# Optimization experiments

Measured on AMD Instinct MI355X. Metric: run time of the kernel, lower is better.

## Reference

```python
import jax, jax.numpy as jnp
import numpy as np


def forward_warp_bilinear(im0, flow):
    # im0: [B,C,H,W], flow: [B,H,W,2] (flow[...,0]=dx, flow[...,1]=dy)
    B, C, H, W = im0.shape
    HW = H * W
    xg = jnp.arange(W, dtype=im0.dtype)
    yg = jnp.arange(H, dtype=im0.dtype)
    x = xg[None, None, :] + flow[..., 0]  # [B,H,W] target x
    y = yg[None, :, None] + flow[..., 1]  # [B,H,W] target y
    x0 = jnp.floor(x)
    y0 = jnp.floor(y)
    x1 = x0 + 1.0
    y1 = y0 + 1.0
    # bilinear splat weights for the 4 neighbours
    w_nw = (x1 - x) * (y1 - y)
    w_ne = (x - x0) * (y1 - y)
    w_sw = (x1 - x) * (y - y0)
    w_se = (x - x0) * (y - y0)
    corners = [(x0, y0, w_nw), (x1, y0, w_ne), (x0, y1, w_sw), (x1, y1, w_se)]
    idx_list, wgt_list = [], []
    for cx, cy, cw in corners:
        xi = cx.astype(jnp.int32)
        yi = cy.astype(jnp.int32)
        valid = (xi >= 0) & (xi < W) & (yi >= 0) & (yi < H)
        flat = jnp.clip(yi, 0, H - 1) * W + jnp.clip(xi, 0, W - 1)  # [B,H,W]
        idx_list.append(flat.reshape(B, HW))
        wgt_list.append(jnp.where(valid, cw, 0.0).reshape(B, HW))
    idx = jnp.concatenate(idx_list, axis=1)  # [B,4*HW]
    wgt = jnp.concatenate(wgt_list, axis=1)  # [B,4*HW]
    src = im0.reshape(B, C, 1, HW)  # source values, tiled over corners
    vals = (src * wgt.reshape(B, 1, 4, HW)).reshape(B, C, 4 * HW)

    def scatter_one(v, i):  # v: [C,4*HW], i: [4*HW]
        return jnp.zeros((C, HW), dtype=v.dtype).at[:, i].add(v)

    out = jax.vmap(scatter_one)(vals, idx)  # [B,C,HW]
    return out.reshape(B, C, H, W)


def setup_inputs() -> dict:
    key = jax.random.key(0)
    k1, k2 = jax.random.split(key)
    B, C, H, W = 8, 16, 512, 512
    im0 = jax.random.normal(k1, (B, C, H, W), dtype=jnp.float32)
    flow = jax.random.normal(k2, (B, H, W, 2), dtype=jnp.float32) * 8.0
    return {"im0": im0, "flow": flow}


def reference(im0, flow):
    return forward_warp_bilinear(im0, flow)
```

## Files before the change

kernel.cpp:

```cpp
#include <hip/hip_runtime.h>


constexpr int B = 8;
constexpr int C = 16;
constexpr int H = 512;
constexpr int W = 512;
constexpr int HW = H * W;

constexpr int T    = 16;
constexpr int R    = 32;
constexpr int TX   = W / T;
constexpr int TY   = H / T;
constexpr int NTILE = B * TX * TY;
constexpr int LCAP = 768;
constexpr int VSTAGE = 400;
constexpr int FARCAP = 1 << 16;
constexpr int NCELL = 289;
constexpr float FARTH = 30.0f;

constexpr size_t WS_CNT  = 0;
constexpr size_t WS_FCNT = 32768;
constexpr size_t WS_FLST = 32896;
constexpr size_t WS_LIST = WS_FLST + (size_t)FARCAP * 8;
constexpr size_t WS_IMT  = (WS_LIST + (size_t)NTILE * LCAP * 2 + 255) & ~(size_t)255;
constexpr size_t IMT_BYTES = (size_t)B * HW * C * 4;

template <bool CL>
__global__ __launch_bounds__(256) void fwarp_prep(
    const float* __restrict__ im0,
    const float* __restrict__ flow,
    float* __restrict__ imT,
    int* __restrict__ cnt,
    int* __restrict__ farcnt,
    int2* __restrict__ farlist,
    unsigned short* __restrict__ list) {

  __shared__ float t[256 * 17];
  const int blk = blockIdx.x;
  const int b   = blk >> 10;
  const int p0  = (blk & 1023) * 256;
  const int tid = threadIdx.x;
  const int lane = tid & 63;
  const int p   = p0 + tid;
  const int idx = (b << 18) + p;

  float v[16];
  if (CL) {
    const float* src = im0 + (size_t)b * C * HW + p0;
    #pragma unroll
    for (int c = 0; c < C; ++c) v[c] = src[(size_t)c * HW + tid];
  }

  float2 f = reinterpret_cast<const float2*>(flow)[idx];
  const int hh = p >> 9, ww = p & (W - 1);

  const bool isfar = (fabsf(f.x) > FARTH || fabsf(f.y) > FARTH);
  if (isfar) {
    unsigned long long m = __ballot(true);
    int ldr = __ffsll((long long)m) - 1;
    int base = 0;
    if (lane == ldr) base = atomicAdd(farcnt, (int)__popcll(m));
    base = __shfl(base, ldr);
    int s = base + (int)__popcll(m & ((1ull << lane) - 1));
    if (s < FARCAP) farlist[s] = make_int2(idx, -1);
  } else {
    float x = (float)ww + f.x;
    float y = (float)hh + f.y;
    int x0 = (int)floorf(x);
    int y0 = (int)floorf(y);

    int txA = ((unsigned)x0       < (unsigned)W) ? (x0 >> 4)       : -1;
    int txB = ((unsigned)(x0 + 1) < (unsigned)W) ? ((x0 + 1) >> 4) : -1;
    if (txB == txA) txB = -1;
    int tyA = ((unsigned)y0       < (unsigned)H) ? (y0 >> 4)       : -1;
    int tyB = ((unsigned)(y0 + 1) < (unsigned)H) ? ((y0 + 1) >> 4) : -1;
    if (tyB == tyA) tyB = -1;

    int clt[4];
    clt[0] = (tyA >= 0 && txA >= 0) ? ((b << 10) | (tyA << 5) | txA) : -1;
    clt[1] = (tyA >= 0 && txB >= 0) ? ((b << 10) | (tyA << 5) | txB) : -1;
    clt[2] = (tyB >= 0 && txA >= 0) ? ((b << 10) | (tyB << 5) | txA) : -1;
    clt[3] = (tyB >= 0 && txB >= 0) ? ((b << 10) | (tyB << 5) | txB) : -1;

    #pragma unroll
    for (int r = 0; r < 4; ++r) {
      int tt = clt[r];
      bool want = (tt >= 0);
      unsigned long long alive = __ballot(want);
      while (alive) {
        int src = __ffsll((long long)alive) - 1;
        int t0  = __shfl(tt, src);
        unsigned long long grp = __ballot(want && tt == t0);
        int base = 0;
        if (lane == src) base = atomicAdd(&cnt[t0], (int)__popcll(grp));
        base = __shfl(base, src);
        if (want && tt == t0) {
          int slot = base + (int)__popcll(grp & ((1ull << lane) - 1));
          int tty = (t0 >> 5) & 31, ttx = t0 & 31;
          int cy = hh - (tty * T - R);
          int cx = ww - (ttx * T - R);
          if (slot < LCAP) {
            list[(size_t)t0 * LCAP + slot] = (unsigned short)((cy << 7) | cx);
          } else {
            int s2 = atomicAdd(farcnt, 1);
            if (s2 < FARCAP) farlist[s2] = make_int2(idx, t0);
          }
          want = false;
        }
        alive &= ~grp;
      }
    }
  }

  if (CL) {
    #pragma unroll
    for (int c = 0; c < C; ++c) t[tid * 17 + c] = v[c];
    __syncthreads();
    float4* dst = reinterpret_cast<float4*>(imT + ((size_t)b * HW + p0) * C);
    #pragma unroll
    for (int i = 0; i < 4; ++i) {
      int k = i * 256 + tid;
      int pp = k >> 2, c4 = (k & 3) * 4;
      const float* tp = &t[pp * 17 + c4];
      dst[k] = make_float4(tp[0], tp[1], tp[2], tp[3]);
    }
  }
}

template <bool CL>
__global__ __launch_bounds__(256, 4) void fwarp_gather(
    const float* __restrict__ im0,
    const float* __restrict__ imT,
    const float* __restrict__ flow,
    float* __restrict__ out,
    const int* __restrict__ cnt,
    const unsigned short* __restrict__ list) {

  __shared__ int            s_cnt[292];
  __shared__ int            s_seg[32];
  __shared__ int            s_start[292];
  __shared__ int            s_p[LCAP];
  __shared__ float2         s_f[LCAP];
  __shared__ unsigned short s_cellid[LCAP];
  __shared__ unsigned short s_ord[LCAP];
  __shared__ float          vch[VSTAGE * 16];

  const int tcx = blockIdx.x, tcy = blockIdx.y, b = blockIdx.z;
  const int tx0 = tcx * T, ty0 = tcy * T;
  const int tid = threadIdx.x;
  const int tile = (b << 10) | (tcy << 5) | tcx;
  const int hy0 = ty0 - R, wx0 = tx0 - R;

  for (int i = tid; i < 292; i += 256) s_cnt[i] = 0;
  __syncthreads();

  const float2* __restrict__ flowv =
      reinterpret_cast<const float2*>(flow) + (size_t)b * HW;
  const int n = min(cnt[tile], LCAP);
  const unsigned short* lp = list + (size_t)tile * LCAP;

  for (int i = tid; i < n; i += 256) {
    int rc = lp[i];
    int hh = hy0 + (rc >> 7);
    int ww = wx0 + (rc & 127);
    int p  = (hh << 9) | ww;
    float2 f = flowv[p];
    float x = (float)ww + f.x, y = (float)hh + f.y;
    float x0f = floorf(x), y0f = floorf(y);
    int cx = (int)x0f - tx0 + 1;
    int cy = (int)y0f - ty0 + 1;
    int cell = ((unsigned)cx <= 16u && (unsigned)cy <= 16u) ? cy * 17 + cx
                                                            : NCELL;
    s_p[i] = p;
    s_f[i] = make_float2(x - x0f, y - y0f);
    s_cellid[i] = (unsigned short)cell;
    atomicAdd(&s_cnt[cell], 1);
  }
  __syncthreads();

  if (tid < 29) {
    int sum = 0;
    #pragma unroll
    for (int j = 0; j < 10; ++j) {
      int ix = tid * 10 + j;
      s_start[ix] = sum;
      sum += s_cnt[ix];
    }
    s_seg[tid] = sum;
  }
  __syncthreads();
  if (tid == 0) {
    int run = 0;
    for (int t2 = 0; t2 < 29; ++t2) { int vv = s_seg[t2]; s_seg[t2] = run; run += vv; }
  }
  __syncthreads();
  for (int i = tid; i < 290; i += 256) s_start[i] += s_seg[i / 10];
  for (int i = tid; i < 292; i += 256) s_cnt[i] = 0;
  __syncthreads();

  for (int i = tid; i < n; i += 256) {
    int cell = s_cellid[i];
    int pos = s_start[cell] + atomicAdd(&s_cnt[cell], 1);
    s_ord[pos] = (unsigned short)i;
  }

  const int nstage = min(n, VSTAGE);
  if (CL) {
    for (int k = tid; k < nstage * 4; k += 256) {
      int i = k >> 2, q = k & 3;
      const float4* s4 = reinterpret_cast<const float4*>(imT) +
                         ((size_t)b * HW + s_p[i]) * 4 + q;
      reinterpret_cast<float4*>(vch)[i * 4 + q] = *s4;
    }
  } else {
    for (int k = tid; k < nstage * 16; k += 256) {
      int i = k >> 4, c = k & 15;
      vch[i * 16 + c] = im0[(size_t)b * C * HW + (size_t)c * HW + s_p[i]];
    }
  }
  __syncthreads();

  float a[16];
  #pragma unroll
  for (int c = 0; c < 16; ++c) a[c] = 0.0f;
  const int lx = tid & 15, ly = tid >> 4;

  #pragma unroll
  for (int k = 0; k < 4; ++k) {
    int cell = (ly + 1 - (k >> 1)) * 17 + (lx + 1 - (k & 1));
    int s = s_start[cell], e = s_start[cell + 1];
    for (int j = s; j < e; ++j) {
      int id = s_ord[j];
      float2 f = s_f[id];
      float wgt = ((k & 1) ? f.x : 1.0f - f.x) * ((k >> 1) ? f.y : 1.0f - f.y);
      if (id < VSTAGE) {
        const float4* vp = reinterpret_cast<const float4*>(vch) + id * 4;
        float4 q0 = vp[0], q1 = vp[1], q2 = vp[2], q3 = vp[3];
        a[0]  += wgt * q0.x; a[1]  += wgt * q0.y;
        a[2]  += wgt * q0.z; a[3]  += wgt * q0.w;
        a[4]  += wgt * q1.x; a[5]  += wgt * q1.y;
        a[6]  += wgt * q1.z; a[7]  += wgt * q1.w;
        a[8]  += wgt * q2.x; a[9]  += wgt * q2.y;
        a[10] += wgt * q2.z; a[11] += wgt * q2.w;
        a[12] += wgt * q3.x; a[13] += wgt * q3.y;
        a[14] += wgt * q3.z; a[15] += wgt * q3.w;
      } else if (CL) {
        const float4* v4 = reinterpret_cast<const float4*>(imT) +
                           ((size_t)b * HW + s_p[id]) * 4;
        float4 q0 = v4[0], q1 = v4[1], q2 = v4[2], q3 = v4[3];
        a[0]  += wgt * q0.x; a[1]  += wgt * q0.y;
        a[2]  += wgt * q0.z; a[3]  += wgt * q0.w;
        a[4]  += wgt * q1.x; a[5]  += wgt * q1.y;
        a[6]  += wgt * q1.z; a[7]  += wgt * q1.w;
        a[8]  += wgt * q2.x; a[9]  += wgt * q2.y;
        a[10] += wgt * q2.z; a[11] += wgt * q2.w;
        a[12] += wgt * q3.x; a[13] += wgt * q3.y;
        a[14] += wgt * q3.z; a[15] += wgt * q3.w;
      } else {
        const float* sp = im0 + (size_t)b * C * HW + s_p[id];
        #pragma unroll
        for (int c = 0; c < 16; ++c) a[c] += wgt * sp[(size_t)c * HW];
      }
    }
  }

  float* ob = out + (size_t)b * C * HW + (size_t)(ty0 + ly) * W + (tx0 + lx);
  #pragma unroll
  for (int c = 0; c < 16; ++c) ob[(size_t)c * HW] = a[c];
}

__global__ __launch_bounds__(256) void fwarp_far(
    const float* __restrict__ im0,
    const float* __restrict__ flow,
    float* __restrict__ out,
    const int* __restrict__ farcnt,
    const int2* __restrict__ farlist) {

  int nf = min(*farcnt, FARCAP);
  for (int i = blockIdx.x * 256 + threadIdx.x; i < nf; i += gridDim.x * 256) {
    int2 ent = farlist[i];
    int idx  = ent.x;
    int tile = ent.y;
    int b  = idx >> 18;
    int p  = idx & (HW - 1);
    int hh = p >> 9, ww = p & (W - 1);
    float2 f = reinterpret_cast<const float2*>(flow)[idx];
    float x = (float)ww + f.x;
    float y = (float)hh + f.y;
    float x0f = floorf(x), y0f = floorf(y);
    int x0 = (int)x0f, y0 = (int)y0f;
    float fx = x - x0f, fy = y - y0f;
    float w00 = (1.0f - fx) * (1.0f - fy), w01 = fx * (1.0f - fy);
    float w10 = (1.0f - fx) * fy,          w11 = fx * fy;

    bool vx0 = (unsigned)x0       < (unsigned)W;
    bool vx1 = (unsigned)(x0 + 1) < (unsigned)W;
    bool vy0 = (unsigned)y0       < (unsigned)H;
    bool vy1 = (unsigned)(y0 + 1) < (unsigned)H;
    if (tile >= 0) {
      int ttx = tile & 31, tty = (tile >> 5) & 31;
      int lx = x0 - ttx * T, ly = y0 - tty * T;
      vx0 &= (unsigned)lx       < (unsigned)T;
      vx1 &= (unsigned)(lx + 1) < (unsigned)T;
      vy0 &= (unsigned)ly       < (unsigned)T;
      vy1 &= (unsigned)(ly + 1) < (unsigned)T;
    }
    bool p00 = vx0 && vy0, p01 = vx1 && vy0, p10 = vx0 && vy1, p11 = vx1 && vy1;
    if (!(p00 | p01 | p10 | p11)) continue;

    int g00 = y0 * W + x0;
    const float* src = im0 + (size_t)b * C * HW + p;
    float* dst = out + (size_t)b * C * HW;
    for (int c = 0; c < C; ++c) {
      float v = src[(size_t)c * HW];
      float* o = dst + (size_t)c * HW;
      if (p00) atomicAdd(o + g00,         v * w00);
      if (p01) atomicAdd(o + g00 + 1,     v * w01);
      if (p10) atomicAdd(o + g00 + W,     v * w10);
      if (p11) atomicAdd(o + g00 + W + 1, v * w11);
    }
  }
}

extern "C" void kernel_launch(void* const* d_in, const int* in_sizes, int n_in,
                              void* d_out, int out_size, void* d_ws, size_t ws_size,
                              hipStream_t stream) {
  const float* im0  = (const float*)d_in[0];
  const float* flow = (const float*)d_in[1];
  float* out = (float*)d_out;

  char* wsb = (char*)d_ws;
  int*            cnt     = (int*)(wsb + WS_CNT);
  int*            farcnt  = (int*)(wsb + WS_FCNT);
  int2*           farlist = (int2*)(wsb + WS_FLST);
  unsigned short* list    = (unsigned short*)(wsb + WS_LIST);
  float*          imT     = (float*)(wsb + WS_IMT);

  const bool useT = ws_size >= WS_IMT + IMT_BYTES;

  hipMemsetAsync(wsb, 0, WS_FLST, stream);

  if (useT)
    fwarp_prep<true><<<8192, 256, 0, stream>>>(im0, flow, imT, cnt, farcnt,
                                               farlist, list);
  else
    fwarp_prep<false><<<8192, 256, 0, stream>>>(im0, flow, imT, cnt, farcnt,
                                                farlist, list);

  dim3 grid(TX, TY, B);
  if (useT)
    fwarp_gather<true><<<grid, 256, 0, stream>>>(im0, imT, flow, out, cnt, list);
  else
    fwarp_gather<false><<<grid, 256, 0, stream>>>(im0, imT, flow, out, cnt, list);

  fwarp_far<<<64, 256, 0, stream>>>(im0, flow, out, farcnt, farlist);
}
```

Baseline: 470.9 us.

## Aggregate tile-list atomics per block and pack flow fractions into list entries

The prep kernel now counts contributions per local tile window in shared memory and does one global atomicAdd per target tile per block, replacing the per-wavefront ballot/shuffle loop. Each list entry becomes a 64-bit word holding the relative position, the floor offset and 16-bit quantized fractional weights, so the gather kernel no longer re-reads flow. The gather kernel sorts the packed entries directly into cell order and stages all source values in LDS (LCAP lowered to 400), with occupancy hint raised to 5. This trades heavier list writes and weight quantization (a small precision risk) for fewer global atomics and a simpler gather loop; more overflow entries may now fall back to the atomic far path.

```diff
diff --git a/kernel.cpp b/kernel.cpp
--- a/kernel.cpp
+++ b/kernel.cpp
@@ -12,17 +12,21 @@
 constexpr int TX   = W / T;
 constexpr int TY   = H / T;
 constexpr int NTILE = B * TX * TY;
-constexpr int LCAP = 768;
-constexpr int VSTAGE = 400;
+constexpr int LCAP = 400;
 constexpr int FARCAP = 1 << 16;
 constexpr int NCELL = 289;
 constexpr float FARTH = 30.0f;
+
+constexpr int LW = 21;
+constexpr int LH = 5;
+constexpr int NLT = LW * LH;
+constexpr int FARSLOT = NLT;
 
 constexpr size_t WS_CNT  = 0;
 constexpr size_t WS_FCNT = 32768;
 constexpr size_t WS_FLST = 32896;
 constexpr size_t WS_LIST = WS_FLST + (size_t)FARCAP * 8;
-constexpr size_t WS_IMT  = (WS_LIST + (size_t)NTILE * LCAP * 2 + 255) & ~(size_t)255;
+constexpr size_t WS_IMT  = (WS_LIST + (size_t)NTILE * LCAP * 8 + 255) & ~(size_t)255;
 constexpr size_t IMT_BYTES = (size_t)B * HW * C * 4;
 
 template <bool CL>
@@ -33,16 +37,21 @@
     int* __restrict__ cnt,
     int* __restrict__ farcnt,
     int2* __restrict__ farlist,
-    unsigned short* __restrict__ list) {
+    unsigned long long* __restrict__ list) {
 
   __shared__ float t[256 * 17];
+  __shared__ int   lcnt[NLT + 1];
+  __shared__ int   lbase[NLT + 1];
+
   const int blk = blockIdx.x;
   const int b   = blk >> 10;
   const int p0  = (blk & 1023) * 256;
   const int tid = threadIdx.x;
-  const int lane = tid & 63;
   const int p   = p0 + tid;
   const int idx = (b << 18) + p;
+  const int hh  = p >> 9, ww = p & (W - 1);
+
+  for (int i = tid; i < NLT + 1; i += 256) lcnt[i] = 0;
 
   float v[16];
   if (CL) {
@@ -52,22 +61,28 @@
   }
 
   float2 f = reinterpret_cast<const float2*>(flow)[idx];
-  const int hh = p >> 9, ww = p & (W - 1);
+  __syncthreads();
+
+  const int tyb = (hh - 31) >> 4;
+  const int txb = ((p0 & (W - 1)) - 31) >> 4;
 
   const bool isfar = (fabsf(f.x) > FARTH || fabsf(f.y) > FARTH);
-  if (isfar) {
-    unsigned long long m = __ballot(true);
-    int ldr = __ffsll((long long)m) - 1;
-    int base = 0;
-    if (lane == ldr) base = atomicAdd(farcnt, (int)__popcll(m));
-    base = __shfl(base, ldr);
-    int s = base + (int)__popcll(m & ((1ull << lane) - 1));
-    if (s < FARCAP) farlist[s] = make_int2(idx, -1);
-  } else {
+
+  int lts[4], tiles[4], rels[4], slots[4];
+  unsigned ehi = 0, elo = 0;
+
+  if (!isfar) {
     float x = (float)ww + f.x;
     float y = (float)hh + f.y;
-    int x0 = (int)floorf(x);
-    int y0 = (int)floorf(y);
+    float x0f = floorf(x), y0f = floorf(y);
+    int x0 = (int)x0f, y0 = (int)y0f;
+    float fx = x - x0f, fy = y - y0f;
+    unsigned fx16 = min((unsigned)(fx * 65536.0f), 65535u);
+    unsigned fy16 = min((unsigned)(fy * 65536.0f), 65535u);
+    ehi = fx16 | (fy16 << 16);
+    int dxe = x0 - ww + 32;
+    int dye = y0 - hh + 32;
+    elo = ((unsigned)dxe << 14) | ((unsigned)dye << 20);
 
     int txA = ((unsigned)x0       < (unsigned)W) ? (x0 >> 4)       : -1;
     int txB = ((unsigned)(x0 + 1) < (unsigned)W) ? ((x0 + 1) >> 4) : -1;
@@ -76,38 +91,57 @@
     int tyB = ((unsigned)(y0 + 1) < (unsigned)H) ? ((y0 + 1) >> 4) : -1;
     if (tyB == tyA) tyB = -1;
 
-    int clt[4];
-    clt[0] = (tyA >= 0 && txA >= 0) ? ((b << 10) | (tyA << 5) | txA) : -1;
-    clt[1] = (tyA >= 0 && txB >= 0) ? ((b << 10) | (tyA << 5) | txB) : -1;
-    clt[2] = (tyB >= 0 && txA >= 0) ? ((b << 10) | (tyB << 5) | txA) : -1;
-    clt[3] = (tyB >= 0 && txB >= 0) ? ((b << 10) | (tyB << 5) | txB) : -1;
-
-    #pragma unroll
-    for (int r = 0; r < 4; ++r) {
-      int tt = clt[r];
-      bool want = (tt >= 0);
-      unsigned long long alive = __ballot(want);
-      while (alive) {
-        int src = __ffsll((long long)alive) - 1;
-        int t0  = __shfl(tt, src);
-        unsigned long long grp = __ballot(want && tt == t0);
-        int base = 0;
-        if (lane == src) base = atomicAdd(&cnt[t0], (int)__popcll(grp));
-        base = __shfl(base, src);
-        if (want && tt == t0) {
-          int slot = base + (int)__popcll(grp & ((1ull << lane) - 1));
-          int tty = (t0 >> 5) & 31, ttx = t0 & 31;
-          int cy = hh - (tty * T - R);
-          int cx = ww - (ttx * T - R);
-          if (slot < LCAP) {
-            list[(size_t)t0 * LCAP + slot] = (unsigned short)((cy << 7) | cx);
-          } else {
-            int s2 = atomicAdd(farcnt, 1);
-            if (s2 < FARCAP) farlist[s2] = make_int2(idx, t0);
-          }
-          want = false;
+    #pragma unroll
+    for (int k = 0; k < 4; ++k) {
+      int ty = (k >> 1) ? tyB : tyA;
+      int tx = (k & 1)  ? txB : txA;
+      bool ok = (ty >= 0) && (tx >= 0);
+      lts[k]   = ok ? (ty - tyb) * LW + (tx - txb) : -1;
+      tiles[k] = (b << 10) | (ty << 5) | tx;
+      rels[k]  = ((hh - (ty * T - R)) << 7) | (ww - (tx * T - R));
+    }
+  } else {
+    #pragma unroll
+    for (int k = 0; k < 4; ++k) lts[k] = -1;
+  }
+
+  int sfar = -1;
+  if (isfar) sfar = atomicAdd(&lcnt[FARSLOT], 1);
+  #pragma unroll
+  for (int k = 0; k < 4; ++k)
+    if (lts[k] >= 0) slots[k] = atomicAdd(&lcnt[lts[k]], 1);
+  __syncthreads();
+
+  if (tid < NLT + 1) {
+    int g = lcnt[tid];
+    if (g > 0) {
+      if (tid == FARSLOT) {
+        lbase[tid] = atomicAdd(farcnt, g);
+      } else {
+        int ty = tyb + tid / LW;
+        int tx = txb + tid % LW;
+        int tile = (b << 10) | (ty << 5) | tx;
+        lbase[tid] = atomicAdd(&cnt[tile], g);
+      }
+    }
+  }
+  __syncthreads();
+
+  if (isfar) {
+    int s = lbase[FARSLOT] + sfar;
+    if (s < FARCAP) farlist[s] = make_int2(idx, -1);
+  } else {
+    #pragma unroll
+    for (int k = 0; k < 4; ++k) {
+      if (lts[k] >= 0) {
+        int slot = lbase[lts[k]] + slots[k];
+        if (slot < LCAP) {
+          list[(size_t)tiles[k] * LCAP + slot] =
+              ((unsigned long long)ehi << 32) | elo | (unsigned)rels[k];
+        } else {
+          int s2 = atomicAdd(farcnt, 1);
+          if (s2 < FARCAP) farlist[s2] = make_int2(idx, tiles[k]);
         }
-        alive &= ~grp;
       }
     }
   }
@@ -128,22 +162,19 @@
 }
 
 template <bool CL>
-__global__ __launch_bounds__(256, 4) void fwarp_gather(
+__global__ __launch_bounds__(256, 5) void fwarp_gather(
     const float* __restrict__ im0,
     const float* __restrict__ imT,
-    const float* __restrict__ flow,
     float* __restrict__ out,
     const int* __restrict__ cnt,
-    const unsigned short* __restrict__ list) {
-
-  __shared__ int            s_cnt[292];
-  __shared__ int            s_seg[32];
-  __shared__ int            s_start[292];
-  __shared__ int            s_p[LCAP];
-  __shared__ float2         s_f[LCAP];
-  __shared__ unsigned short s_cellid[LCAP];
-  __shared__ unsigned short s_ord[LCAP];
-  __shared__ float          vch[VSTAGE * 16];
+    const unsigned long long* __restrict__ list) {
+
+  __shared__ int      s_cnt[290];
+  __shared__ int      s_start[290];
+  __shared__ int      s_seg[29];
+  __shared__ unsigned s_code[LCAP];
+  __shared__ unsigned s_fq[LCAP];
+  __shared__ float    vch[LCAP * 16];
 
   const int tcx = blockIdx.x, tcy = blockIdx.y, b = blockIdx.z;
   const int tx0 = tcx * T, ty0 = tcy * T;
@@ -151,30 +182,31 @@
   const int tile = (b << 10) | (tcy << 5) | tcx;
   const int hy0 = ty0 - R, wx0 = tx0 - R;
 
-  for (int i = tid; i < 292; i += 256) s_cnt[i] = 0;
-  __syncthreads();
-
-  const float2* __restrict__ flowv =
-      reinterpret_cast<const float2*>(flow) + (size_t)b * HW;
+  for (int i = tid; i < 290; i += 256) s_cnt[i] = 0;
+  __syncthreads();
+
   const int n = min(cnt[tile], LCAP);
-  const unsigned short* lp = list + (size_t)tile * LCAP;
-
-  for (int i = tid; i < n; i += 256) {
-    int rc = lp[i];
-    int hh = hy0 + (rc >> 7);
-    int ww = wx0 + (rc & 127);
-    int p  = (hh << 9) | ww;
-    float2 f = flowv[p];
-    float x = (float)ww + f.x, y = (float)hh + f.y;
-    float x0f = floorf(x), y0f = floorf(y);
-    int cx = (int)x0f - tx0 + 1;
-    int cy = (int)y0f - ty0 + 1;
-    int cell = ((unsigned)cx <= 16u && (unsigned)cy <= 16u) ? cy * 17 + cx
-                                                            : NCELL;
-    s_p[i] = p;
-    s_f[i] = make_float2(x - x0f, y - y0f);
-    s_cellid[i] = (unsigned short)cell;
-    atomicAdd(&s_cnt[cell], 1);
+  const unsigned long long* lp = list + (size_t)tile * LCAP;
+
+  unsigned lo[2], hi[2];
+  int cell[2];
+  #pragma unroll
+  for (int r = 0; r < 2; ++r) {
+    int i = tid + r * 256;
+    cell[r] = -1;
+    if (i < n) {
+      unsigned long long e = lp[i];
+      lo[r] = (unsigned)e;
+      hi[r] = (unsigned)(e >> 32);
+      int rel = lo[r] & 0x3fff;
+      int dxe = (lo[r] >> 14) & 63;
+      int dye = (lo[r] >> 20) & 63;
+      int cx = (rel & 127) + dxe - 63;
+      int cy = (rel >> 7)  + dye - 63;
+      cell[r] = ((unsigned)cx <= 16u && (unsigned)cy <= 16u) ? cy * 17 + cx
+                                                             : NCELL;
+      atomicAdd(&s_cnt[cell[r]], 1);
+    }
   }
   __syncthreads();
 
@@ -195,27 +227,34 @@
   }
   __syncthreads();
   for (int i = tid; i < 290; i += 256) s_start[i] += s_seg[i / 10];
-  for (int i = tid; i < 292; i += 256) s_cnt[i] = 0;
-  __syncthreads();
-
-  for (int i = tid; i < n; i += 256) {
-    int cell = s_cellid[i];
-    int pos = s_start[cell] + atomicAdd(&s_cnt[cell], 1);
-    s_ord[pos] = (unsigned short)i;
-  }
-
-  const int nstage = min(n, VSTAGE);
+  for (int i = tid; i < 290; i += 256) s_cnt[i] = 0;
+  __syncthreads();
+
+  #pragma unroll
+  for (int r = 0; r < 2; ++r) {
+    if (cell[r] >= 0) {
+      int pos = s_start[cell[r]] + atomicAdd(&s_cnt[cell[r]], 1);
+      s_code[pos] = lo[r];
+      s_fq[pos]   = hi[r];
+    }
+  }
+  __syncthreads();
+
   if (CL) {
-    for (int k = tid; k < nstage * 4; k += 256) {
+    for (int k = tid; k < n * 4; k += 256) {
       int i = k >> 2, q = k & 3;
+      int rel = s_code[i] & 0x3fff;
+      int p = ((hy0 + (rel >> 7)) << 9) | (wx0 + (rel & 127));
       const float4* s4 = reinterpret_cast<const float4*>(imT) +
-                         ((size_t)b * HW + s_p[i]) * 4 + q;
+                         ((size_t)b * HW + p) * 4 + q;
       reinterpret_cast<float4*>(vch)[i * 4 + q] = *s4;
     }
   } else {
-    for (int k = tid; k < nstage * 16; k += 256) {
+    for (int k = tid; k < n * 16; k += 256) {
       int i = k >> 4, c = k & 15;
-      vch[i * 16 + c] = im0[(size_t)b * C * HW + (size_t)c * HW + s_p[i]];
+      int rel = s_code[i] & 0x3fff;
+      int p = ((hy0 + (rel >> 7)) << 9) | (wx0 + (rel & 127));
+      vch[i * 16 + c] = im0[(size_t)b * C * HW + (size_t)c * HW + p];
     }
   }
   __syncthreads();
@@ -227,40 +266,24 @@
 
   #pragma unroll
   for (int k = 0; k < 4; ++k) {
-    int cell = (ly + 1 - (k >> 1)) * 17 + (lx + 1 - (k & 1));
-    int s = s_start[cell], e = s_start[cell + 1];
+    int cell2 = (ly + 1 - (k >> 1)) * 17 + (lx + 1 - (k & 1));
+    int s = s_start[cell2];
+    int e = (cell2 < 289) ? s_start[cell2 + 1] : n;
     for (int j = s; j < e; ++j) {
-      int id = s_ord[j];
-      float2 f = s_f[id];
-      float wgt = ((k & 1) ? f.x : 1.0f - f.x) * ((k >> 1) ? f.y : 1.0f - f.y);
-      if (id < VSTAGE) {
-        const float4* vp = reinterpret_cast<const float4*>(vch) + id * 4;
-        float4 q0 = vp[0], q1 = vp[1], q2 = vp[2], q3 = vp[3];
-        a[0]  += wgt * q0.x; a[1]  += wgt * q0.y;
-        a[2]  += wgt * q0.z; a[3]  += wgt * q0.w;
-        a[4]  += wgt * q1.x; a[5]  += wgt * q1.y;
-        a[6]  += wgt * q1.z; a[7]  += wgt * q1.w;
-        a[8]  += wgt * q2.x; a[9]  += wgt * q2.y;
-        a[10] += wgt * q2.z; a[11] += wgt * q2.w;
-        a[12] += wgt * q3.x; a[13] += wgt * q3.y;
-        a[14] += wgt * q3.z; a[15] += wgt * q3.w;
-      } else if (CL) {
-        const float4* v4 = reinterpret_cast<const float4*>(imT) +
-                           ((size_t)b * HW + s_p[id]) * 4;
-        float4 q0 = v4[0], q1 = v4[1], q2 = v4[2], q3 = v4[3];
-        a[0]  += wgt * q0.x; a[1]  += wgt * q0.y;
-        a[2]  += wgt * q0.z; a[3]  += wgt * q0.w;
-        a[4]  += wgt * q1.x; a[5]  += wgt * q1.y;
-        a[6]  += wgt * q1.z; a[7]  += wgt * q1.w;
-        a[8]  += wgt * q2.x; a[9]  += wgt * q2.y;
-        a[10] += wgt * q2.z; a[11] += wgt * q2.w;
-        a[12] += wgt * q3.x; a[13] += wgt * q3.y;
-        a[14] += wgt * q3.z; a[15] += wgt * q3.w;
-      } else {
-        const float* sp = im0 + (size_t)b * C * HW + s_p[id];
-        #pragma unroll
-        for (int c = 0; c < 16; ++c) a[c] += wgt * sp[(size_t)c * HW];
-      }
+      unsigned fq = s_fq[j];
+      float fx = (float)(fq & 0xffffu) * (1.0f / 65536.0f);
+      float fy = (float)(fq >> 16)     * (1.0f / 65536.0f);
+      float wgt = ((k & 1) ? fx : 1.0f - fx) * ((k >> 1) ? fy : 1.0f - fy);
+      const float4* vp = reinterpret_cast<const float4*>(vch) + j * 4;
+      float4 q0 = vp[0], q1 = vp[1], q2 = vp[2], q3 = vp[3];
+      a[0]  += wgt * q0.x; a[1]  += wgt * q0.y;
+      a[2]  += wgt * q0.z; a[3]  += wgt * q0.w;
+      a[4]  += wgt * q1.x; a[5]  += wgt * q1.y;
+      a[6]  += wgt * q1.z; a[7]  += wgt * q1.w;
+      a[8]  += wgt * q2.x; a[9]  += wgt * q2.y;
+      a[10] += wgt * q2.z; a[11] += wgt * q2.w;
+      a[12] += wgt * q3.x; a[13] += wgt * q3.y;
+      a[14] += wgt * q3.z; a[15] += wgt * q3.w;
     }
   }
 
@@ -330,11 +353,11 @@
   float* out = (float*)d_out;
 
   char* wsb = (char*)d_ws;
-  int*            cnt     = (int*)(wsb + WS_CNT);
-  int*            farcnt  = (int*)(wsb + WS_FCNT);
-  int2*           farlist = (int2*)(wsb + WS_FLST);
-  unsigned short* list    = (unsigned short*)(wsb + WS_LIST);
-  float*          imT     = (float*)(wsb + WS_IMT);
+  int*                cnt     = (int*)(wsb + WS_CNT);
+  int*                farcnt  = (int*)(wsb + WS_FCNT);
+  int2*               farlist = (int2*)(wsb + WS_FLST);
+  unsigned long long* list    = (unsigned long long*)(wsb + WS_LIST);
+  float*              imT     = (float*)(wsb + WS_IMT);
 
   const bool useT = ws_size >= WS_IMT + IMT_BYTES;
 
@@ -349,9 +372,9 @@
 
   dim3 grid(TX, TY, B);
   if (useT)
-    fwarp_gather<true><<<grid, 256, 0, stream>>>(im0, imT, flow, out, cnt, list);
+    fwarp_gather<true><<<grid, 256, 0, stream>>>(im0, imT, out, cnt, list);
   else
-    fwarp_gather<false><<<grid, 256, 0, stream>>>(im0, imT, flow, out, cnt, list);
+    fwarp_gather<false><<<grid, 256, 0, stream>>>(im0, imT, out, cnt, list);
 
   fwarp_far<<<64, 256, 0, stream>>>(im0, flow, out, farcnt, farlist);
 }
```

Result: faster. 385.8 us (-18.1%).
